# Kernel optimization log

Measured on AMD Instinct MI355X. Metric: run time of the kernel, lower is better.

Reference implementation:

```python
import jax, jax.numpy as jnp
import numpy as np

N = 50000    # nodes
E = 800000   # edges per block
D = 128      # embed_dim
H = 8        # heads
DH = D // H  # head dim
L = 2        # layers / blocks
IN = 128     # in_feats
P = 8192     # pos/neg pairs
FF = 2 * D   # FFN hidden
NEG_SLOPE = 0.2


def layer_norm(x, g, b, eps=1e-5):
    m = x.mean(-1, keepdims=True)
    v = ((x - m) ** 2).mean(-1, keepdims=True)
    return (x - m) / jnp.sqrt(v + eps) * g + b


def setup_inputs() -> dict:
    key = jax.random.key(0)
    ks = jax.random.split(key, 32)
    f32 = jnp.float32
    def w(k, shape, fan_in):
        return jax.random.normal(k, shape, f32) * (1.0 / np.sqrt(fan_in))
    inp = {
        'x': jax.random.normal(ks[0], (N, IN), f32),
        'src': jax.random.randint(ks[1], (L, E), 0, N),
        'dst': jax.random.randint(ks[2], (L, E), 0, N),
        'pos_src': jax.random.randint(ks[3], (P,), 0, N),
        'pos_dst': jax.random.randint(ks[4], (P,), 0, N),
        'neg_src': jax.random.randint(ks[5], (P,), 0, N),
        'neg_dst': jax.random.randint(ks[6], (P,), 0, N),
        # input projection
        'W_in': w(ks[7], (IN, D), IN), 'b_in': jnp.zeros((D,), f32),
        # per-layer attention weights, stacked over L
        'Wq': w(ks[8], (L, D, D), D), 'bq': jnp.zeros((L, D), f32),
        'Wk': w(ks[9], (L, D, D), D), 'bk': jnp.zeros((L, D), f32),
        'Wv': w(ks[10], (L, D, D), D), 'bv': jnp.zeros((L, D), f32),
        'Wo': w(ks[11], (L, D, D), D), 'bo': jnp.zeros((L, D), f32),
        'ln1_g': jnp.ones((L, D), f32), 'ln1_b': jnp.zeros((L, D), f32),
        'Wf1': w(ks[12], (L, D, FF), D), 'bf1': jnp.zeros((L, FF), f32),
        'Wf2': w(ks[13], (L, FF, D), FF), 'bf2': jnp.zeros((L, D), f32),
        'ln2_g': jnp.ones((L, D), f32), 'ln2_b': jnp.zeros((L, D), f32),
        # predictor MLP: D -> D//2 -> 1
        'Wp1': w(ks[14], (D, D // 2), D), 'bp1': jnp.zeros((D // 2,), f32),
        'Wp2': w(ks[15], (D // 2, 1), D // 2), 'bp2': jnp.zeros((1,), f32),
    }
    return inp


def reference(x, src, dst, pos_src, pos_dst, neg_src, neg_dst,
              W_in, b_in, Wq, bq, Wk, bk, Wv, bv, Wo, bo,
              ln1_g, ln1_b, Wf1, bf1, Wf2, bf2, ln2_g, ln2_b,
              Wp1, bp1, Wp2, bp2):
    scale = 1.0 / np.sqrt(DH)
    h = x @ W_in + b_in  # [N, D] (dropout is identity in eval mode)
    for l in range(L):
        s_l, d_l = src[l], dst[l]
        q = (h @ Wq[l] + bq[l]).reshape(N, H, DH)
        k = (h @ Wk[l] + bk[l]).reshape(N, H, DH)
        v = (h @ Wv[l] + bv[l]).reshape(N, H, DH)
        # per-edge attention scores [E, H]
        sc = jnp.einsum('ehd,ehd->eh', q[d_l], k[s_l]) * scale
        # segment softmax over incoming edges of each dst node
        m = jax.ops.segment_max(sc, d_l, num_segments=N)   # [N, H]
        ex = jnp.exp(sc - m[d_l])
        den = jax.ops.segment_sum(ex, d_l, num_segments=N)  # [N, H]
        alpha = ex / (den[d_l] + 1e-9)
        agg = jax.ops.segment_sum(alpha[..., None] * v[s_l], d_l,
                                  num_segments=N).reshape(N, D)
        h = layer_norm(h + agg @ Wo[l] + bo[l], ln1_g[l], ln1_b[l])
        ff = jax.nn.relu(h @ Wf1[l] + bf1[l]) @ Wf2[l] + bf2[l]
        h = layer_norm(h + ff, ln2_g[l], ln2_b[l])

    def predict(a, b):
        z = h[a] * h[b]  # gather-multiply edge scoring
        z = jax.nn.leaky_relu(z @ Wp1 + bp1, NEG_SLOPE)
        return z @ Wp2 + bp2  # [P, 1]

    pos_score = predict(pos_src, pos_dst)
    neg_score = predict(neg_src, neg_dst)
    return (pos_score, neg_score, h)
```

## Files before the change

### kernel.cpp

```cpp
#include <hip/hip_runtime.h>
#include <hip/hip_bf16.h>
#include <math.h>

#define N_NODES 50000
#define NE      800000
#define D       128
#define H       8
#define DH      16
#define NLAYER  2
#define IN_F    128
#define PP      8192
#define FF      256
#define MPAD    50048
#define CAP     96
#define NBIN    196
#define BCAP    48
#define GCAP    4608
#define CHUNK   2048

typedef short  bf16x8 __attribute__((ext_vector_type(8)));
typedef float  f32x4  __attribute__((ext_vector_type(4)));
typedef __hip_bfloat16 bf16;
typedef unsigned short u16;
typedef unsigned int   u32;

__device__ __forceinline__ float bflo(u32 u) { return __uint_as_float(u << 16); }
__device__ __forceinline__ float bfhi(u32 u) { return __uint_as_float(u & 0xffff0000u); }

__global__ __launch_bounds__(256) void bin_kernel(
    const int* __restrict__ dst, const int* __restrict__ src,
    u32* __restrict__ gbin, int* __restrict__ gbin_cnt)
{
    __shared__ u32 ent[NBIN * BCAP];
    __shared__ int bcnt[NBIN];
    const int t = threadIdx.x, l = blockIdx.y;
    const int base = blockIdx.x * CHUNK;
    if (t < NBIN) bcnt[t] = 0;
    __syncthreads();
    #pragma unroll
    for (int j = 0; j < CHUNK / 256; j++) {
        int e = base + j * 256 + t;
        if (e < NE) {
            int d = dst[(size_t)l * NE + e];
            int s = src[(size_t)l * NE + e];
            int bin = d >> 8;
            int slot = atomicAdd(&bcnt[bin], 1);
            if (slot < BCAP) ent[bin * BCAP + slot] = ((u32)s << 16) | (u32)(d & 255);
        }
    }
    __syncthreads();
    if (t < NBIN) {
        int c = bcnt[t]; if (c > BCAP) c = BCAP;
        if (c > 0) {
            int gb = atomicAdd(&gbin_cnt[l * NBIN + t], c);
            u32* gp = gbin + ((size_t)l * NBIN + t) * GCAP;
            for (int i = 0; i < c; i++)
                if (gb + i < GCAP) gp[gb + i] = ent[t * BCAP + i];
        }
    }
}

__global__ __launch_bounds__(256) void expand_kernel(
    const u32* __restrict__ gbin, const int* __restrict__ gbin_cnt,
    int* __restrict__ cnt, u16* __restrict__ ssrc)
{
    __shared__ int lcnt[256];
    const int t = threadIdx.x, b = blockIdx.x, l = blockIdx.y;
    lcnt[t] = 0;
    __syncthreads();
    int n = gbin_cnt[l * NBIN + b]; if (n > GCAP) n = GCAP;
    const u32* gp = gbin + ((size_t)l * NBIN + b) * GCAP;
    for (int i = t; i < n; i += 256) {
        u32 u = gp[i];
        int dl = (int)(u & 255);
        int pos = atomicAdd(&lcnt[dl], 1);
        if (pos < CAP) {
            int d = (b << 8) + dl;
            ssrc[((size_t)l * N_NODES + d) * CAP + pos] = (u16)(u >> 16);
        }
    }
    __syncthreads();
    int d = (b << 8) + t;
    if (d < N_NODES) cnt[l * N_NODES + d] = lcnt[t];
}

__global__ void xb_kernel(const float* __restrict__ x, bf16* __restrict__ xb) {
    int id = blockIdx.x * blockDim.x + threadIdx.x;
    if (id >= MPAD * IN_F) return;
    int r = id / IN_F;
    xb[id] = __float2bfloat16(r < N_NODES ? x[id] : 0.f);
}

__global__ void prep_kernel(const float* __restrict__ W_in,
                            const float* __restrict__ Wq, const float* __restrict__ Wk,
                            const float* __restrict__ Wv, const float* __restrict__ Wo,
                            const float* __restrict__ Wf1, const float* __restrict__ Wf2,
                            const float* __restrict__ bq, const float* __restrict__ bk,
                            const float* __restrict__ bv,
                            bf16* __restrict__ win_t, bf16* __restrict__ wqkv_t,
                            bf16* __restrict__ wo_t, bf16* __restrict__ wf1_t,
                            bf16* __restrict__ wf2_t, float* __restrict__ bqkv)
{
    int id = blockIdx.x * blockDim.x + threadIdx.x;
    if (id < 16384) {
        int n = id >> 7, k = id & 127;
        win_t[id] = __float2bfloat16(W_in[k * 128 + n]);
        return;
    }
    id -= 16384;
    if (id < NLAYER * 49152) {
        int l = id / 49152, j = id % 49152;
        int r = j >> 7, k = j & 127;
        const float* Ws; int col;
        if (r < 128) { Ws = Wq; col = r; }
        else {
            int u = r - 128, hh = u >> 5, w = u & 31;
            if (w < 16) { Ws = Wk; col = hh * 16 + w; }
            else        { Ws = Wv; col = hh * 16 + w - 16; }
        }
        wqkv_t[(size_t)l * 49152 + j] = __float2bfloat16(Ws[(size_t)l * 16384 + k * 128 + col]);
        return;
    }
    id -= NLAYER * 49152;
    if (id < NLAYER * 16384) {
        int l = id / 16384, j = id % 16384;
        int n = j >> 7, k = j & 127;
        wo_t[id] = __float2bfloat16(Wo[(size_t)l * 16384 + k * 128 + n]);
        return;
    }
    id -= NLAYER * 16384;
    if (id < NLAYER * 32768) {
        int l = id / 32768, j = id % 32768;
        int n = j >> 7, k = j & 127;
        wf1_t[id] = __float2bfloat16(Wf1[(size_t)l * 32768 + k * 256 + n]);
        return;
    }
    id -= NLAYER * 32768;
    if (id < NLAYER * 32768) {
        int l = id / 32768, j = id % 32768;
        int n = j >> 8, k = j & 255;
        wf2_t[id] = __float2bfloat16(Wf2[(size_t)l * 32768 + k * 128 + n]);
        return;
    }
    id -= NLAYER * 32768;
    if (id < NLAYER * 384) {
        int l = id / 384, r = id % 384;
        float v;
        if (r < 128) v = bq[l * 128 + r];
        else {
            int u = r - 128, hh = u >> 5, w = u & 31;
            v = (w < 16) ? bk[l * 128 + hh * 16 + w] : bv[l * 128 + hh * 16 + w - 16];
        }
        bqkv[l * 384 + r] = v;
    }
}

__global__ __launch_bounds__(256) void gemm_mfma(
    const bf16* __restrict__ A, const bf16* __restrict__ Wt,
    const float* __restrict__ bias,
    float* __restrict__ Cf, bf16* __restrict__ Cb,
    int Mvalid, int K, int Nc, int lda, int relu)
{
    __shared__ float4 As4[1024];
    __shared__ float4 Bs4[1024];
    char* As = (char*)As4;
    char* Bs = (char*)Bs4;
    const int t = threadIdx.x;
    const int wave = t >> 6, lane = t & 63;
    const int wr = wave >> 1, wc = wave & 1;
    const int r0 = blockIdx.x * 128, c0 = blockIdx.y * 128;

    f32x4 acc[4][4] = {};

    const int lrow   = t >> 3;
    const int lcol16 = (t & 7) * 16;

    for (int k0 = 0; k0 < K; k0 += 64) {
        #pragma unroll
        for (int p = 0; p < 4; p++) {
            int row = p * 32 + lrow;
            float4 av = *(const float4*)((const char*)(A  + (size_t)(r0 + row) * lda + k0) + lcol16);
            float4 bv = *(const float4*)((const char*)(Wt + (size_t)(c0 + row) * K + k0) + lcol16);
            int sw = lcol16 ^ ((row & 7) << 4);
            *(float4*)(As + row * 128 + sw) = av;
            *(float4*)(Bs + row * 128 + sw) = bv;
        }
        __syncthreads();
        #pragma unroll
        for (int kk = 0; kk < 2; kk++) {
            bf16x8 af[4], bfr[4];
            int kbyte = kk * 64 + (lane >> 4) * 16;
            #pragma unroll
            for (int m = 0; m < 4; m++) {
                int rowa = wr * 64 + m * 16 + (lane & 15);
                af[m]  = *(const bf16x8*)(As + rowa * 128 + (kbyte ^ ((rowa & 7) << 4)));
                int rowb = wc * 64 + m * 16 + (lane & 15);
                bfr[m] = *(const bf16x8*)(Bs + rowb * 128 + (kbyte ^ ((rowb & 7) << 4)));
            }
            #pragma unroll
            for (int m = 0; m < 4; m++)
                #pragma unroll
                for (int n = 0; n < 4; n++)
                    acc[m][n] = __builtin_amdgcn_mfma_f32_16x16x32_bf16(af[m], bfr[n], acc[m][n], 0, 0, 0);
        }
        __syncthreads();
    }

    const int colbase = c0 + wc * 64 + (lane & 15);
    const int rowbase = r0 + wr * 64 + ((lane >> 4) << 2);
    #pragma unroll
    for (int n = 0; n < 4; n++) {
        int col = colbase + n * 16;
        float bsv = bias[col];
        #pragma unroll
        for (int m = 0; m < 4; m++) {
            #pragma unroll
            for (int i = 0; i < 4; i++) {
                int row = rowbase + m * 16 + i;
                if (row < Mvalid) {
                    float v = acc[m][n][i] + bsv;
                    if (relu) v = fmaxf(v, 0.f);
                    if (Cf) Cf[(size_t)row * Nc + col] = v;
                    if (Cb) Cb[(size_t)row * Nc + col] = __float2bfloat16(v);
                }
            }
        }
    }
}

__global__ __launch_bounds__(256) void tail_fused(
    const bf16* __restrict__ qkv,
    const bf16* __restrict__ wo_t,
    const float* __restrict__ bo,
    const float* __restrict__ g1, const float* __restrict__ be1,
    const bf16* __restrict__ Wf1t,
    const float* __restrict__ b1,
    const bf16* __restrict__ Wf2t,
    const float* __restrict__ b2,
    const float* __restrict__ g2, const float* __restrict__ be2,
    float* __restrict__ h, bf16* __restrict__ hb)
{
    __shared__ char lds[81920];
    char* AsA = lds;
    char* Ah1 = lds;
    char* Xs  = lds + 16384;
    char* Bs  = lds + 49152;
    const int t = threadIdx.x;
    const int w = t >> 6, lane = t & 63;
    const int r0 = blockIdx.x * 64;
    const int c = lane & 15, sub = lane >> 4;

    f32x4 acc0[8] = {};
    #pragma unroll
    for (int k0 = 0; k0 < 128; k0 += 64) {
        {
            int row = t >> 2;
            int c16 = (t & 3) * 32;
            const char* ap = (const char*)(qkv + (size_t)(r0 + row) * 384 + k0);
            float4 a0 = *(const float4*)(ap + c16);
            float4 a1 = *(const float4*)(ap + c16 + 16);
            *(float4*)(AsA + row * 128 + ((c16)      ^ ((row & 7) << 4))) = a0;
            *(float4*)(AsA + row * 128 + ((c16 + 16) ^ ((row & 7) << 4))) = a1;
        }
        {
            int row = t >> 1;
            int c16 = (t & 1) * 64;
            const char* bp = (const char*)(wo_t + (size_t)row * 128 + k0);
            #pragma unroll
            for (int j = 0; j < 4; j++) {
                float4 b = *(const float4*)(bp + c16 + j * 16);
                *(float4*)(Bs + row * 128 + ((c16 + j * 16) ^ ((row & 7) << 4))) = b;
            }
        }
        __syncthreads();
        #pragma unroll
        for (int kk = 0; kk < 2; kk++) {
            int kbyte = kk * 64 + sub * 16;
            int rowa = w * 16 + c;
            bf16x8 af = *(const bf16x8*)(AsA + rowa * 128 + (kbyte ^ ((rowa & 7) << 4)));
            #pragma unroll
            for (int n = 0; n < 8; n++) {
                int rowb = n * 16 + c;
                bf16x8 bf8 = *(const bf16x8*)(Bs + rowb * 128 + (kbyte ^ ((rowb & 7) << 4)));
                acc0[n] = __builtin_amdgcn_mfma_f32_16x16x32_bf16(af, bf8, acc0[n], 0, 0, 0);
            }
        }
        __syncthreads();
    }

    float h1v[8][4];
    {
        float bsv[8], gv[8], bev[8];
        #pragma unroll
        for (int n = 0; n < 8; n++) {
            int col = n * 16 + c;
            bsv[n] = bo[col]; gv[n] = g1[col]; bev[n] = be1[col];
        }
        #pragma unroll
        for (int i = 0; i < 4; i++) {
            int row = r0 + w * 16 + sub * 4 + i;
            bool ok = row < N_NODES;
            float x[8];
            float s = 0.f;
            #pragma unroll
            for (int n = 0; n < 8; n++) {
                float res = ok ? h[(size_t)row * D + n * 16 + c] : 0.f;
                x[n] = res + acc0[n][i] + bsv[n];
                s += x[n];
            }
            s += __shfl_xor(s, 1); s += __shfl_xor(s, 2);
            s += __shfl_xor(s, 4); s += __shfl_xor(s, 8);
            float mean = s * (1.f / 128.f);
            float v = 0.f;
            #pragma unroll
            for (int n = 0; n < 8; n++) { float dd = x[n] - mean; v += dd * dd; }
            v += __shfl_xor(v, 1); v += __shfl_xor(v, 2);
            v += __shfl_xor(v, 4); v += __shfl_xor(v, 8);
            float rstd = rsqrtf(v * (1.f / 128.f) + 1e-5f);
            int lrow = w * 16 + sub * 4 + i;
            #pragma unroll
            for (int n = 0; n < 8; n++) {
                float o = (x[n] - mean) * rstd * gv[n] + bev[n];
                h1v[n][i] = o;
                int byte = (n * 16 + c) * 2;
                int addr = lrow * 256 + ((byte & ~15) ^ ((lrow & 7) << 4)) + (byte & 15);
                *(bf16*)(Ah1 + addr) = __float2bfloat16(o);
            }
        }
    }
    __syncthreads();

    f32x4 acc1[16] = {};
    #pragma unroll
    for (int kc = 0; kc < 2; kc++) {
        {
            int row = t;
            const char* bp = (const char*)Wf1t + row * 256 + kc * 128;
            #pragma unroll
            for (int j = 0; j < 8; j++) {
                float4 v = *(const float4*)(bp + j * 16);
                *(float4*)(Bs + row * 128 + ((j * 16) ^ ((row & 7) << 4))) = v;
            }
        }
        __syncthreads();
        #pragma unroll
        for (int kkl = 0; kkl < 2; kkl++) {
            int abyte = (kc * 2 + kkl) * 64 + sub * 16;
            int rowa = w * 16 + c;
            bf16x8 af = *(const bf16x8*)(Ah1 + rowa * 256 + (abyte ^ ((rowa & 7) << 4)));
            int bbyte = kkl * 64 + sub * 16;
            #pragma unroll
            for (int n = 0; n < 16; n++) {
                int rowb = n * 16 + c;
                bf16x8 bf8 = *(const bf16x8*)(Bs + rowb * 128 + (bbyte ^ ((rowb & 7) << 4)));
                acc1[n] = __builtin_amdgcn_mfma_f32_16x16x32_bf16(af, bf8, acc1[n], 0, 0, 0);
            }
        }
        __syncthreads();
    }

    #pragma unroll
    for (int n = 0; n < 16; n++) {
        float bs = b1[n * 16 + c];
        #pragma unroll
        for (int i = 0; i < 4; i++) {
            int row = w * 16 + sub * 4 + i;
            float v = fmaxf(acc1[n][i] + bs, 0.f);
            int byte = (n * 16 + c) * 2;
            int addr = row * 512 + ((byte & ~15) ^ ((row & 7) << 4)) + (byte & 15);
            *(bf16*)(Xs + addr) = __float2bfloat16(v);
        }
    }
    __syncthreads();

    f32x4 acc2[8] = {};
    #pragma unroll
    for (int kc = 0; kc < 2; kc++) {
        {
            int row = t >> 1;
            int off = (t & 1) * 128;
            const char* bp = (const char*)Wf2t + row * 512 + kc * 256 + off;
            #pragma unroll
            for (int j = 0; j < 8; j++) {
                float4 v = *(const float4*)(bp + j * 16);
                *(float4*)(Bs + row * 256 + ((off + j * 16) ^ ((row & 7) << 4))) = v;
            }
        }
        __syncthreads();
        #pragma unroll
        for (int kkl = 0; kkl < 4; kkl++) {
            int xbyte = kc * 256 + kkl * 64 + sub * 16;
            int rowa = w * 16 + c;
            bf16x8 af = *(const bf16x8*)(Xs + rowa * 512 + (xbyte ^ ((rowa & 7) << 4)));
            int bbyte = kkl * 64 + sub * 16;
            #pragma unroll
            for (int n = 0; n < 8; n++) {
                int rowb = n * 16 + c;
                bf16x8 bf8 = *(const bf16x8*)(Bs + rowb * 256 + (bbyte ^ ((rowb & 7) << 4)));
                acc2[n] = __builtin_amdgcn_mfma_f32_16x16x32_bf16(af, bf8, acc2[n], 0, 0, 0);
            }
        }
        __syncthreads();
    }

    {
        float bsv[8], gv[8], bev[8];
        #pragma unroll
        for (int n = 0; n < 8; n++) {
            int col = n * 16 + c;
            bsv[n] = b2[col]; gv[n] = g2[col]; bev[n] = be2[col];
        }
        #pragma unroll
        for (int i = 0; i < 4; i++) {
            int row = r0 + w * 16 + sub * 4 + i;
            bool ok = row < N_NODES;
            float x[8];
            float s = 0.f;
            #pragma unroll
            for (int n = 0; n < 8; n++) {
                x[n] = h1v[n][i] + acc2[n][i] + bsv[n];
                s += x[n];
            }
            s += __shfl_xor(s, 1); s += __shfl_xor(s, 2);
            s += __shfl_xor(s, 4); s += __shfl_xor(s, 8);
            float mean = s * (1.f / 128.f);
            float v = 0.f;
            #pragma unroll
            for (int n = 0; n < 8; n++) { float dd = x[n] - mean; v += dd * dd; }
            v += __shfl_xor(v, 1); v += __shfl_xor(v, 2);
            v += __shfl_xor(v, 4); v += __shfl_xor(v, 8);
            float rstd = rsqrtf(v * (1.f / 128.f) + 1e-5f);
            if (ok) {
                #pragma unroll
                for (int n = 0; n < 8; n++) {
                    float o = (x[n] - mean) * rstd * gv[n] + bev[n];
                    h [(size_t)row * D + n * 16 + c] = o;
                    hb[(size_t)row * D + n * 16 + c] = __float2bfloat16(o);
                }
            }
        }
    }
}

__global__ __launch_bounds__(256) void attn_fused(
    const bf16* __restrict__ qkv,
    const int* __restrict__ cnt, const u16* __restrict__ ssrc,
    bf16* __restrict__ aggout)
{
    const float S2 = 0.25f * 1.44269504088896f;
    int wid = threadIdx.x >> 6, lane = threadIdx.x & 63;
    int d = blockIdx.x * 4 + wid;
    if (d >= N_NODES) return;
    int slot = lane >> 3, h = lane & 7;

    const u32* qr = (const u32*)(qkv + (size_t)d * 384 + h * DH);
    float qf[16];
    {
        uint4 q0 = *(const uint4*)(qr);
        uint4 q1 = *(const uint4*)(qr + 4);
        qf[0]=bflo(q0.x); qf[1]=bfhi(q0.x); qf[2]=bflo(q0.y); qf[3]=bfhi(q0.y);
        qf[4]=bflo(q0.z); qf[5]=bfhi(q0.z); qf[6]=bflo(q0.w); qf[7]=bfhi(q0.w);
        qf[8]=bflo(q1.x); qf[9]=bfhi(q1.x); qf[10]=bflo(q1.y); qf[11]=bfhi(q1.y);
        qf[12]=bflo(q1.z); qf[13]=bfhi(q1.z); qf[14]=bflo(q1.w); qf[15]=bfhi(q1.w);
    }

    int deg = cnt[d];
    if (deg > CAP) deg = CAP;
    const u16* bp = ssrc + (size_t)d * CAP;
    float m2 = -INFINITY, den = 0.f;
    float acc[16] = {};

    for (int i = slot; i < deg; i += 8) {
        int s = bp[i];
        const uint4* kvp = (const uint4*)(qkv + (size_t)s * 384 + 128 + h * 32);
        uint4 k0 = kvp[0], k1 = kvp[1], v0 = kvp[2], v1 = kvp[3];
        float p = qf[0]*bflo(k0.x) + qf[1]*bfhi(k0.x)
                + qf[2]*bflo(k0.y) + qf[3]*bfhi(k0.y)
                + qf[4]*bflo(k0.z) + qf[5]*bfhi(k0.z)
                + qf[6]*bflo(k0.w) + qf[7]*bfhi(k0.w)
                + qf[8]*bflo(k1.x) + qf[9]*bfhi(k1.x)
                + qf[10]*bflo(k1.y) + qf[11]*bfhi(k1.y)
                + qf[12]*bflo(k1.z) + qf[13]*bfhi(k1.z)
                + qf[14]*bflo(k1.w) + qf[15]*bfhi(k1.w);
        float p2 = p * S2;
        float w;
        if (p2 > m2 + 8.f) {
            float f = exp2f(m2 - p2);
            den *= f;
            #pragma unroll
            for (int j = 0; j < 16; j++) acc[j] *= f;
            m2 = p2;
            w = 1.f;
        } else {
            w = exp2f(p2 - m2);
        }
        den += w;
        acc[0]  += w*bflo(v0.x); acc[1]  += w*bfhi(v0.x);
        acc[2]  += w*bflo(v0.y); acc[3]  += w*bfhi(v0.y);
        acc[4]  += w*bflo(v0.z); acc[5]  += w*bfhi(v0.z);
        acc[6]  += w*bflo(v0.w); acc[7]  += w*bfhi(v0.w);
        acc[8]  += w*bflo(v1.x); acc[9]  += w*bfhi(v1.x);
        acc[10] += w*bflo(v1.y); acc[11] += w*bfhi(v1.y);
        acc[12] += w*bflo(v1.z); acc[13] += w*bfhi(v1.z);
        acc[14] += w*bflo(v1.w); acc[15] += w*bfhi(v1.w);
    }

    #pragma unroll
    for (int o = 8; o < 64; o <<= 1) {
        float om   = __shfl_xor(m2, o);
        float oden = __shfl_xor(den, o);
        float M = fmaxf(m2, om);
        float fa = (m2 > -INFINITY) ? exp2f(m2 - M) : 0.f;
        float fb = (om > -INFINITY) ? exp2f(om - M) : 0.f;
        den = den * fa + oden * fb;
        #pragma unroll
        for (int j = 0; j < 16; j++) {
            float oa = __shfl_xor(acc[j], o);
            acc[j] = acc[j] * fa + oa * fb;
        }
        m2 = M;
    }

    float r = 1.f / (den + 1e-9f);
    float o0 = 0.f, o1 = 0.f;
    #pragma unroll
    for (int j = 0; j < 8; j++) {
        if (slot == j) { o0 = acc[2 * j]; o1 = acc[2 * j + 1]; }
    }
    bf16* op = aggout + (size_t)d * 384 + h * DH + slot * 2;
    op[0] = __float2bfloat16(o0 * r);
    op[1] = __float2bfloat16(o1 * r);
}

__global__ void predict_kernel(const float* __restrict__ h,
                               const int* __restrict__ ps, const int* __restrict__ pd,
                               const int* __restrict__ ns, const int* __restrict__ nd,
                               const float* __restrict__ Wp1, const float* __restrict__ bp1,
                               const float* __restrict__ Wp2, const float* __restrict__ bp2,
                               float* __restrict__ out)
{
    __shared__ float z[128];
    int p = blockIdx.x;
    int a, b;
    if (p < PP) { a = ps[p]; b = pd[p]; }
    else        { a = ns[p - PP]; b = nd[p - PP]; }
    int t = threadIdx.x;
    z[t]      = h[(size_t)a * D + t]      * h[(size_t)b * D + t];
    z[t + 64] = h[(size_t)a * D + t + 64] * h[(size_t)b * D + t + 64];
    __syncthreads();
    float acc = bp1[t];
    #pragma unroll 4
    for (int i = 0; i < 128; i++) acc += z[i] * Wp1[(size_t)i * 64 + t];
    acc = acc > 0.f ? acc : 0.2f * acc;
    float part = acc * Wp2[t];
    #pragma unroll
    for (int o = 32; o > 0; o >>= 1) part += __shfl_down(part, o);
    if (t == 0) out[p] = part + bp2[0];
}

extern "C" void kernel_launch(void* const* d_in, const int* in_sizes, int n_in,
                              void* d_out, int out_size, void* d_ws, size_t ws_size,
                              hipStream_t stream)
{
    const float* x       = (const float*)d_in[0];
    const int*   src     = (const int*)d_in[1];
    const int*   dst     = (const int*)d_in[2];
    const int*   pos_src = (const int*)d_in[3];
    const int*   pos_dst = (const int*)d_in[4];
    const int*   neg_src = (const int*)d_in[5];
    const int*   neg_dst = (const int*)d_in[6];
    const float* W_in = (const float*)d_in[7];
    const float* b_in = (const float*)d_in[8];
    const float* Wq = (const float*)d_in[9];
    const float* bq = (const float*)d_in[10];
    const float* Wk = (const float*)d_in[11];
    const float* bk = (const float*)d_in[12];
    const float* Wv = (const float*)d_in[13];
    const float* bv = (const float*)d_in[14];
    const float* Wo = (const float*)d_in[15];
    const float* bo = (const float*)d_in[16];
    const float* ln1g = (const float*)d_in[17];
    const float* ln1b = (const float*)d_in[18];
    const float* Wf1 = (const float*)d_in[19];
    const float* bf1 = (const float*)d_in[20];
    const float* Wf2 = (const float*)d_in[21];
    const float* bf2 = (const float*)d_in[22];
    const float* ln2g = (const float*)d_in[23];
    const float* ln2b = (const float*)d_in[24];
    const float* Wp1 = (const float*)d_in[25];
    const float* bp1 = (const float*)d_in[26];
    const float* Wp2 = (const float*)d_in[27];
    const float* bp2 = (const float*)d_in[28];

    float* out = (float*)d_out;
    float* h   = out + 2 * PP;

    bf16* B    = (bf16*)d_ws;
    bf16* qkvb = B;
    bf16* xb   = B;
    bf16* hb   = B + (size_t)MPAD * 384;
    int*  cnt  = (int*)(hb + (size_t)MPAD * 128);
    u16*  ssrc = (u16*)(cnt + 2 * N_NODES);
    bf16* wtb  = (bf16*)(ssrc + (size_t)2 * N_NODES * CAP);
    bf16* win_t  = wtb;
    bf16* wqkv_t = wtb + 16384;
    bf16* wo_t   = wtb + 16384 + 98304;
    bf16* wf1_t  = wtb + 16384 + 98304 + 32768;
    bf16* wf2_t  = wtb + 16384 + 98304 + 32768 + 65536;
    float* bqkv  = (float*)(wtb + 16384 + 98304 + 32768 + 65536 + 65536);
    int*  gbin_cnt = (int*)(bqkv + NLAYER * 384);
    u32*  gbin     = (u32*)(gbin_cnt + 2 * NBIN);

    auto cdiv = [](int a, int b) { return (a + b - 1) / b; };
    const int GX = MPAD / 128;
    const int GL = MPAD / 64;

    xb_kernel<<<cdiv(MPAD * IN_F, 256), 256, 0, stream>>>(x, xb);
    prep_kernel<<<1091, 256, 0, stream>>>(W_in, Wq, Wk, Wv, Wo, Wf1, Wf2, bq, bk, bv,
                                          win_t, wqkv_t, wo_t, wf1_t, wf2_t, bqkv);

    (void)hipMemsetAsync(gbin_cnt, 0, 2 * NBIN * sizeof(int), stream);
    bin_kernel<<<dim3(cdiv(NE, CHUNK), 2), 256, 0, stream>>>(dst, src, gbin, gbin_cnt);
    expand_kernel<<<dim3(NBIN, 2), 256, 0, stream>>>(gbin, gbin_cnt, cnt, ssrc);

    gemm_mfma<<<dim3(GX, 1), 256, 0, stream>>>(xb, win_t, b_in, h, hb, N_NODES, 128, 128, 128, 0);

    for (int l = 0; l < NLAYER; l++) {
        gemm_mfma<<<dim3(GX, 3), 256, 0, stream>>>(hb, wqkv_t + l * 49152, bqkv + l * 384,
                                                   nullptr, qkvb, N_NODES, 128, 384, 128, 0);

        attn_fused<<<cdiv(N_NODES, 4), 256, 0, stream>>>(qkvb, cnt + l * N_NODES,
                                                         ssrc + (size_t)l * N_NODES * CAP, qkvb);

        tail_fused<<<GL, 256, 0, stream>>>(qkvb, wo_t + l * 16384, bo + l * D,
                                           ln1g + l * D, ln1b + l * D,
                                           wf1_t + l * 32768, bf1 + l * FF,
                                           wf2_t + l * 32768, bf2 + l * D,
                                           ln2g + l * D, ln2b + l * D, h, hb);
    }

    predict_kernel<<<2 * PP, 64, 0, stream>>>(h, pos_src, pos_dst, neg_src, neg_dst,
                                              Wp1, bp1, Wp2, bp2, out);
}
```

Baseline: 362.0 us.

## Fuse input projection and QKV GEMMs into head and tail kernels

Adds a head kernel that converts x to bf16 in LDS, runs the input projection, and feeds the result straight into the layer-0 QKV projection. The tail kernel now computes the next layer's QKV from its LayerNorm output held in LDS. This removes the x-to-bf16 pass, the hb round trip through global memory and the standalone QKV GEMM launches. It also folds the bin-count memset into the prep kernel. The trade-off is more serial work and LDS per block, and the tail kernel now overwrites the qkv buffer it also reads from.

```diff
diff --git a/kernel.cpp b/kernel.cpp
--- a/kernel.cpp
+++ b/kernel.cpp
@@ -26,6 +26,7 @@
 
 __device__ __forceinline__ float bflo(u32 u) { return __uint_as_float(u << 16); }
 __device__ __forceinline__ float bfhi(u32 u) { return __uint_as_float(u & 0xffff0000u); }
+__device__ __forceinline__ u16 bfbits(float f) { bf16 t = __float2bfloat16(f); return *(u16*)&t; }
 
 __global__ __launch_bounds__(256) void bin_kernel(
     const int* __restrict__ dst, const int* __restrict__ src,
@@ -84,13 +85,6 @@
     if (d < N_NODES) cnt[l * N_NODES + d] = lcnt[t];
 }
 
-__global__ void xb_kernel(const float* __restrict__ x, bf16* __restrict__ xb) {
-    int id = blockIdx.x * blockDim.x + threadIdx.x;
-    if (id >= MPAD * IN_F) return;
-    int r = id / IN_F;
-    xb[id] = __float2bfloat16(r < N_NODES ? x[id] : 0.f);
-}
-
 __global__ void prep_kernel(const float* __restrict__ W_in,
                             const float* __restrict__ Wq, const float* __restrict__ Wk,
                             const float* __restrict__ Wv, const float* __restrict__ Wo,
@@ -99,7 +93,8 @@
                             const float* __restrict__ bv,
                             bf16* __restrict__ win_t, bf16* __restrict__ wqkv_t,
                             bf16* __restrict__ wo_t, bf16* __restrict__ wf1_t,
-                            bf16* __restrict__ wf2_t, float* __restrict__ bqkv)
+                            bf16* __restrict__ wf2_t, float* __restrict__ bqkv,
+                            int* __restrict__ gbin_cnt)
 {
     int id = blockIdx.x * blockDim.x + threadIdx.x;
     if (id < 16384) {
@@ -152,79 +147,127 @@
             v = (w < 16) ? bk[l * 128 + hh * 16 + w] : bv[l * 128 + hh * 16 + w - 16];
         }
         bqkv[l * 384 + r] = v;
-    }
+        return;
+    }
+    id -= NLAYER * 384;
+    if (id < 2 * NBIN) gbin_cnt[id] = 0;
 }
 
-__global__ __launch_bounds__(256) void gemm_mfma(
-    const bf16* __restrict__ A, const bf16* __restrict__ Wt,
-    const float* __restrict__ bias,
-    float* __restrict__ Cf, bf16* __restrict__ Cb,
-    int Mvalid, int K, int Nc, int lda, int relu)
+__global__ __launch_bounds__(256) void head_fused(
+    const float* __restrict__ x, const bf16* __restrict__ win_t,
+    const float* __restrict__ b_in,
+    const bf16* __restrict__ wqkv0, const float* __restrict__ bqkv0,
+    float* __restrict__ h, bf16* __restrict__ qkvb)
 {
-    __shared__ float4 As4[1024];
-    __shared__ float4 Bs4[1024];
-    char* As = (char*)As4;
-    char* Bs = (char*)Bs4;
+    __shared__ char lds[65536];
+    char* Axb = lds;
+    char* Hb  = lds + 16384;
+    char* Bs  = lds + 32768;
     const int t = threadIdx.x;
-    const int wave = t >> 6, lane = t & 63;
-    const int wr = wave >> 1, wc = wave & 1;
-    const int r0 = blockIdx.x * 128, c0 = blockIdx.y * 128;
-
-    f32x4 acc[4][4] = {};
-
-    const int lrow   = t >> 3;
-    const int lcol16 = (t & 7) * 16;
-
-    for (int k0 = 0; k0 < K; k0 += 64) {
-        #pragma unroll
-        for (int p = 0; p < 4; p++) {
-            int row = p * 32 + lrow;
-            float4 av = *(const float4*)((const char*)(A  + (size_t)(r0 + row) * lda + k0) + lcol16);
-            float4 bv = *(const float4*)((const char*)(Wt + (size_t)(c0 + row) * K + k0) + lcol16);
-            int sw = lcol16 ^ ((row & 7) << 4);
-            *(float4*)(As + row * 128 + sw) = av;
-            *(float4*)(Bs + row * 128 + sw) = bv;
+    const int w = t >> 6, lane = t & 63;
+    const int r0 = blockIdx.x * 64;
+    const int c = lane & 15, sub = lane >> 4;
+
+    {
+        int row = t >> 2;
+        int col0 = (t & 3) * 32;
+        int grow = r0 + row;
+        #pragma unroll
+        for (int j = 0; j < 8; j++) {
+            float4 v = make_float4(0.f, 0.f, 0.f, 0.f);
+            if (grow < N_NODES) v = *(const float4*)(x + (size_t)grow * 128 + col0 + j * 4);
+            u32 lo = ((u32)bfbits(v.y) << 16) | bfbits(v.x);
+            u32 hi = ((u32)bfbits(v.w) << 16) | bfbits(v.z);
+            int byte = (col0 + j * 4) * 2;
+            int addr = row * 256 + ((byte & ~15) ^ ((row & 7) << 4)) + (byte & 15);
+            *(u32*)(Axb + addr)     = lo;
+            *(u32*)(Axb + addr + 4) = hi;
+        }
+    }
+    {
+        int row = t >> 1;
+        int off = (t & 1) * 128;
+        const char* bp = (const char*)win_t + row * 256 + off;
+        #pragma unroll
+        for (int j = 0; j < 8; j++) {
+            float4 v = *(const float4*)(bp + j * 16);
+            *(float4*)(Bs + row * 256 + ((off + j * 16) ^ ((row & 7) << 4))) = v;
+        }
+    }
+    __syncthreads();
+
+    f32x4 acc0[8] = {};
+    #pragma unroll
+    for (int kc = 0; kc < 2; kc++) {
+        #pragma unroll
+        for (int kk = 0; kk < 2; kk++) {
+            int kbyte = (kc * 2 + kk) * 64 + sub * 16;
+            int rowa = w * 16 + c;
+            bf16x8 af = *(const bf16x8*)(Axb + rowa * 256 + (kbyte ^ ((rowa & 7) << 4)));
+            #pragma unroll
+            for (int n = 0; n < 8; n++) {
+                int rowb = n * 16 + c;
+                bf16x8 bf8 = *(const bf16x8*)(Bs + rowb * 256 + (kbyte ^ ((rowb & 7) << 4)));
+                acc0[n] = __builtin_amdgcn_mfma_f32_16x16x32_bf16(af, bf8, acc0[n], 0, 0, 0);
+            }
+        }
+    }
+
+    #pragma unroll
+    for (int i = 0; i < 4; i++) {
+        int lrow = w * 16 + sub * 4 + i;
+        int grow = r0 + lrow;
+        bool ok = grow < N_NODES;
+        #pragma unroll
+        for (int n = 0; n < 8; n++) {
+            float v = acc0[n][i] + b_in[n * 16 + c];
+            if (ok) h[(size_t)grow * D + n * 16 + c] = v;
+            int byte = (n * 16 + c) * 2;
+            int addr = lrow * 256 + ((byte & ~15) ^ ((lrow & 7) << 4)) + (byte & 15);
+            *(u16*)(Hb + addr) = bfbits(v);
+        }
+    }
+    __syncthreads();
+
+    #pragma unroll
+    for (int cc = 0; cc < 3; cc++) {
+        {
+            int row = t >> 1;
+            int off = (t & 1) * 128;
+            const char* bp = (const char*)wqkv0 + (size_t)(cc * 128 + row) * 256 + off;
+            #pragma unroll
+            for (int j = 0; j < 8; j++) {
+                float4 v = *(const float4*)(bp + j * 16);
+                *(float4*)(Bs + row * 256 + ((off + j * 16) ^ ((row & 7) << 4))) = v;
+            }
         }
         __syncthreads();
-        #pragma unroll
-        for (int kk = 0; kk < 2; kk++) {
-            bf16x8 af[4], bfr[4];
-            int kbyte = kk * 64 + (lane >> 4) * 16;
-            #pragma unroll
-            for (int m = 0; m < 4; m++) {
-                int rowa = wr * 64 + m * 16 + (lane & 15);
-                af[m]  = *(const bf16x8*)(As + rowa * 128 + (kbyte ^ ((rowa & 7) << 4)));
-                int rowb = wc * 64 + m * 16 + (lane & 15);
-                bfr[m] = *(const bf16x8*)(Bs + rowb * 128 + (kbyte ^ ((rowb & 7) << 4)));
-            }
-            #pragma unroll
-            for (int m = 0; m < 4; m++)
+        f32x4 acc[8] = {};
+        #pragma unroll
+        for (int kc = 0; kc < 2; kc++) {
+            #pragma unroll
+            for (int kk = 0; kk < 2; kk++) {
+                int kbyte = (kc * 2 + kk) * 64 + sub * 16;
+                int rowa = w * 16 + c;
+                bf16x8 af = *(const bf16x8*)(Hb + rowa * 256 + (kbyte ^ ((rowa & 7) << 4)));
                 #pragma unroll
-                for (int n = 0; n < 4; n++)
-                    acc[m][n] = __builtin_amdgcn_mfma_f32_16x16x32_bf16(af[m], bfr[n], acc[m][n], 0, 0, 0);
+                for (int n = 0; n < 8; n++) {
+                    int rowb = n * 16 + c;
+                    bf16x8 bf8 = *(const bf16x8*)(Bs + rowb * 256 + (kbyte ^ ((rowb & 7) << 4)));
+                    acc[n] = __builtin_amdgcn_mfma_f32_16x16x32_bf16(af, bf8, acc[n], 0, 0, 0);
+                }
+            }
+        }
+        #pragma unroll
+        for (int i = 0; i < 4; i++) {
+            int grow = r0 + w * 16 + sub * 4 + i;
+            #pragma unroll
+            for (int n = 0; n < 8; n++) {
+                int col = cc * 128 + n * 16 + c;
+                qkvb[(size_t)grow * 384 + col] = __float2bfloat16(acc[n][i] + bqkv0[col]);
+            }
         }
         __syncthreads();
-    }
-
-    const int colbase = c0 + wc * 64 + (lane & 15);
-    const int rowbase = r0 + wr * 64 + ((lane >> 4) << 2);
-    #pragma unroll
-    for (int n = 0; n < 4; n++) {
-        int col = colbase + n * 16;
-        float bsv = bias[col];
-        #pragma unroll
-        for (int m = 0; m < 4; m++) {
-            #pragma unroll
-            for (int i = 0; i < 4; i++) {
-                int row = rowbase + m * 16 + i;
-                if (row < Mvalid) {
-                    float v = acc[m][n][i] + bsv;
-                    if (relu) v = fmaxf(v, 0.f);
-                    if (Cf) Cf[(size_t)row * Nc + col] = v;
-                    if (Cb) Cb[(size_t)row * Nc + col] = __float2bfloat16(v);
-                }
-            }
-        }
     }
 }
 
@@ -238,7 +281,9 @@
     const bf16* __restrict__ Wf2t,
     const float* __restrict__ b2,
     const float* __restrict__ g2, const float* __restrict__ be2,
-    float* __restrict__ h, bf16* __restrict__ hb)
+    float* __restrict__ h,
+    const bf16* __restrict__ wqkv_next, const float* __restrict__ bqkv_next,
+    bf16* __restrict__ qkvb_out)
 {
     __shared__ char lds[81920];
     char* AsA = lds;
@@ -324,7 +369,7 @@
                 h1v[n][i] = o;
                 int byte = (n * 16 + c) * 2;
                 int addr = lrow * 256 + ((byte & ~15) ^ ((lrow & 7) << 4)) + (byte & 15);
-                *(bf16*)(Ah1 + addr) = __float2bfloat16(o);
+                *(u16*)(Ah1 + addr) = bfbits(o);
             }
         }
     }
@@ -368,7 +413,7 @@
             float v = fmaxf(acc1[n][i] + bs, 0.f);
             int byte = (n * 16 + c) * 2;
             int addr = row * 512 + ((byte & ~15) ^ ((row & 7) << 4)) + (byte & 15);
-            *(bf16*)(Xs + addr) = __float2bfloat16(v);
+            *(u16*)(Xs + addr) = bfbits(v);
         }
     }
     __syncthreads();
@@ -412,8 +457,9 @@
         }
         #pragma unroll
         for (int i = 0; i < 4; i++) {
-            int row = r0 + w * 16 + sub * 4 + i;
-            bool ok = row < N_NODES;
+            int lrow = w * 16 + sub * 4 + i;
+            int grow = r0 + lrow;
+            bool ok = grow < N_NODES;
             float x[8];
             float s = 0.f;
             #pragma unroll
@@ -430,14 +476,57 @@
             v += __shfl_xor(v, 1); v += __shfl_xor(v, 2);
             v += __shfl_xor(v, 4); v += __shfl_xor(v, 8);
             float rstd = rsqrtf(v * (1.f / 128.f) + 1e-5f);
-            if (ok) {
+            #pragma unroll
+            for (int n = 0; n < 8; n++) {
+                float o = (x[n] - mean) * rstd * gv[n] + bev[n];
+                if (ok) h[(size_t)grow * D + n * 16 + c] = o;
+                int byte = (n * 16 + c) * 2;
+                int addr = lrow * 256 + ((byte & ~15) ^ ((lrow & 7) << 4)) + (byte & 15);
+                *(u16*)(Xs + addr) = bfbits(o);
+            }
+        }
+    }
+
+    if (wqkv_next) {
+        #pragma unroll
+        for (int cc = 0; cc < 3; cc++) {
+            {
+                int row = t >> 1;
+                int off = (t & 1) * 128;
+                const char* bp = (const char*)wqkv_next + (size_t)(cc * 128 + row) * 256 + off;
+                #pragma unroll
+                for (int j = 0; j < 8; j++) {
+                    float4 v = *(const float4*)(bp + j * 16);
+                    *(float4*)(Bs + row * 256 + ((off + j * 16) ^ ((row & 7) << 4))) = v;
+                }
+            }
+            __syncthreads();
+            f32x4 acc[8] = {};
+            #pragma unroll
+            for (int kc = 0; kc < 2; kc++) {
+                #pragma unroll
+                for (int kk = 0; kk < 2; kk++) {
+                    int kbyte = (kc * 2 + kk) * 64 + sub * 16;
+                    int rowa = w * 16 + c;
+                    bf16x8 af = *(const bf16x8*)(Xs + rowa * 256 + (kbyte ^ ((rowa & 7) << 4)));
+                    #pragma unroll
+                    for (int n = 0; n < 8; n++) {
+                        int rowb = n * 16 + c;
+                        bf16x8 bf8 = *(const bf16x8*)(Bs + rowb * 256 + (kbyte ^ ((rowb & 7) << 4)));
+                        acc[n] = __builtin_amdgcn_mfma_f32_16x16x32_bf16(af, bf8, acc[n], 0, 0, 0);
+                    }
+                }
+            }
+            #pragma unroll
+            for (int i = 0; i < 4; i++) {
+                int grow = r0 + w * 16 + sub * 4 + i;
                 #pragma unroll
                 for (int n = 0; n < 8; n++) {
-                    float o = (x[n] - mean) * rstd * gv[n] + bev[n];
-                    h [(size_t)row * D + n * 16 + c] = o;
-                    hb[(size_t)row * D + n * 16 + c] = __float2bfloat16(o);
+                    int col = cc * 128 + n * 16 + c;
+                    qkvb_out[(size_t)grow * 384 + col] = __float2bfloat16(acc[n][i] + bqkv_next[col]);
                 }
             }
+            __syncthreads();
         }
     }
 }
@@ -597,9 +686,7 @@
 
     bf16* B    = (bf16*)d_ws;
     bf16* qkvb = B;
-    bf16* xb   = B;
-    bf16* hb   = B + (size_t)MPAD * 384;
-    int*  cnt  = (int*)(hb + (size_t)MPAD * 128);
+    int*  cnt  = (int*)(B + (size_t)MPAD * 384);
     u16*  ssrc = (u16*)(cnt + 2 * N_NODES);
     bf16* wtb  = (bf16*)(ssrc + (size_t)2 * N_NODES * CAP);
     bf16* win_t  = wtb;
@@ -612,31 +699,26 @@
     u32*  gbin     = (u32*)(gbin_cnt + 2 * NBIN);
 
     auto cdiv = [](int a, int b) { return (a + b - 1) / b; };
-    const int GX = MPAD / 128;
     const int GL = MPAD / 64;
 
-    xb_kernel<<<cdiv(MPAD * IN_F, 256), 256, 0, stream>>>(x, xb);
-    prep_kernel<<<1091, 256, 0, stream>>>(W_in, Wq, Wk, Wv, Wo, Wf1, Wf2, bq, bk, bv,
-                                          win_t, wqkv_t, wo_t, wf1_t, wf2_t, bqkv);
-
-    (void)hipMemsetAsync(gbin_cnt, 0, 2 * NBIN * sizeof(int), stream);
+    prep_kernel<<<1093, 256, 0, stream>>>(W_in, Wq, Wk, Wv, Wo, Wf1, Wf2, bq, bk, bv,
+                                          win_t, wqkv_t, wo_t, wf1_t, wf2_t, bqkv, gbin_cnt);
     bin_kernel<<<dim3(cdiv(NE, CHUNK), 2), 256, 0, stream>>>(dst, src, gbin, gbin_cnt);
     expand_kernel<<<dim3(NBIN, 2), 256, 0, stream>>>(gbin, gbin_cnt, cnt, ssrc);
 
-    gemm_mfma<<<dim3(GX, 1), 256, 0, stream>>>(xb, win_t, b_in, h, hb, N_NODES, 128, 128, 128, 0);
+    head_fused<<<GL, 256, 0, stream>>>(x, win_t, b_in, wqkv_t, bqkv, h, qkvb);
 
     for (int l = 0; l < NLAYER; l++) {
-        gemm_mfma<<<dim3(GX, 3), 256, 0, stream>>>(hb, wqkv_t + l * 49152, bqkv + l * 384,
-                                                   nullptr, qkvb, N_NODES, 128, 384, 128, 0);
-
         attn_fused<<<cdiv(N_NODES, 4), 256, 0, stream>>>(qkvb, cnt + l * N_NODES,
                                                          ssrc + (size_t)l * N_NODES * CAP, qkvb);
-
+        const bf16* wnext  = (l + 1 < NLAYER) ? (wqkv_t + (l + 1) * 49152) : nullptr;
+        const float* bnext = (l + 1 < NLAYER) ? (bqkv + (l + 1) * 384) : nullptr;
         tail_fused<<<GL, 256, 0, stream>>>(qkvb, wo_t + l * 16384, bo + l * D,
                                            ln1g + l * D, ln1b + l * D,
                                            wf1_t + l * 32768, bf1 + l * FF,
                                            wf2_t + l * 32768, bf2 + l * D,
-                                           ln2g + l * D, ln2b + l * D, h, hb);
+                                           ln2g + l * D, ln2b + l * D, h,
+                                           wnext, bnext, qkvb);
     }
 
     predict_kernel<<<2 * PP, 64, 0, stream>>>(h, pos_src, pos_dst, neg_src, neg_dst,
```

Result: slower. 406.9 us (+12.4%).

## Split FFN hidden dimension into halves to shrink tail kernel LDS footprint

Applied to the files above, without the earlier changes.

The fused tail kernel's FFN now processes the 256-wide hidden layer in two 128-column halves. Each half is computed, passed through ReLU, and immediately accumulated into the second GEMM, so the hidden-activation buffer and weight staging buffers shrink and total LDS drops from 80 KB to 48 KB. This is meant to allow more resident blocks per CU, at the cost of more barriers and smaller weight tiles per stage. Separately, the gbin_cnt memset is folded into prep_kernel to remove one API call.

```diff
diff --git a/kernel.cpp b/kernel.cpp
--- a/kernel.cpp
+++ b/kernel.cpp
@@ -26,6 +26,7 @@
 
 __device__ __forceinline__ float bflo(u32 u) { return __uint_as_float(u << 16); }
 __device__ __forceinline__ float bfhi(u32 u) { return __uint_as_float(u & 0xffff0000u); }
+__device__ __forceinline__ u16 bfbits(float f) { bf16 t = __float2bfloat16(f); return *(u16*)&t; }
 
 __global__ __launch_bounds__(256) void bin_kernel(
     const int* __restrict__ dst, const int* __restrict__ src,
@@ -99,7 +100,8 @@
                             const float* __restrict__ bv,
                             bf16* __restrict__ win_t, bf16* __restrict__ wqkv_t,
                             bf16* __restrict__ wo_t, bf16* __restrict__ wf1_t,
-                            bf16* __restrict__ wf2_t, float* __restrict__ bqkv)
+                            bf16* __restrict__ wf2_t, float* __restrict__ bqkv,
+                            int* __restrict__ gbin_cnt)
 {
     int id = blockIdx.x * blockDim.x + threadIdx.x;
     if (id < 16384) {
@@ -152,7 +154,10 @@
             v = (w < 16) ? bk[l * 128 + hh * 16 + w] : bv[l * 128 + hh * 16 + w - 16];
         }
         bqkv[l * 384 + r] = v;
-    }
+        return;
+    }
+    id -= NLAYER * 384;
+    if (id < 2 * NBIN) gbin_cnt[id] = 0;
 }
 
 __global__ __launch_bounds__(256) void gemm_mfma(
@@ -240,11 +245,11 @@
     const float* __restrict__ g2, const float* __restrict__ be2,
     float* __restrict__ h, bf16* __restrict__ hb)
 {
-    __shared__ char lds[81920];
+    __shared__ char lds[49152];
     char* AsA = lds;
     char* Ah1 = lds;
     char* Xs  = lds + 16384;
-    char* Bs  = lds + 49152;
+    char* Bs  = lds + 32768;
     const int t = threadIdx.x;
     const int w = t >> 6, lane = t & 63;
     const int r0 = blockIdx.x * 64;
@@ -324,83 +329,84 @@
                 h1v[n][i] = o;
                 int byte = (n * 16 + c) * 2;
                 int addr = lrow * 256 + ((byte & ~15) ^ ((lrow & 7) << 4)) + (byte & 15);
-                *(bf16*)(Ah1 + addr) = __float2bfloat16(o);
-            }
-        }
-    }
-    __syncthreads();
-
-    f32x4 acc1[16] = {};
-    #pragma unroll
-    for (int kc = 0; kc < 2; kc++) {
-        {
-            int row = t;
-            const char* bp = (const char*)Wf1t + row * 256 + kc * 128;
-            #pragma unroll
-            for (int j = 0; j < 8; j++) {
-                float4 v = *(const float4*)(bp + j * 16);
-                *(float4*)(Bs + row * 128 + ((j * 16) ^ ((row & 7) << 4))) = v;
-            }
-        }
-        __syncthreads();
-        #pragma unroll
-        for (int kkl = 0; kkl < 2; kkl++) {
-            int abyte = (kc * 2 + kkl) * 64 + sub * 16;
-            int rowa = w * 16 + c;
-            bf16x8 af = *(const bf16x8*)(Ah1 + rowa * 256 + (abyte ^ ((rowa & 7) << 4)));
-            int bbyte = kkl * 64 + sub * 16;
-            #pragma unroll
-            for (int n = 0; n < 16; n++) {
-                int rowb = n * 16 + c;
-                bf16x8 bf8 = *(const bf16x8*)(Bs + rowb * 128 + (bbyte ^ ((rowb & 7) << 4)));
-                acc1[n] = __builtin_amdgcn_mfma_f32_16x16x32_bf16(af, bf8, acc1[n], 0, 0, 0);
-            }
-        }
-        __syncthreads();
-    }
-
-    #pragma unroll
-    for (int n = 0; n < 16; n++) {
-        float bs = b1[n * 16 + c];
-        #pragma unroll
-        for (int i = 0; i < 4; i++) {
-            int row = w * 16 + sub * 4 + i;
-            float v = fmaxf(acc1[n][i] + bs, 0.f);
-            int byte = (n * 16 + c) * 2;
-            int addr = row * 512 + ((byte & ~15) ^ ((row & 7) << 4)) + (byte & 15);
-            *(bf16*)(Xs + addr) = __float2bfloat16(v);
+                *(u16*)(Ah1 + addr) = bfbits(o);
+            }
         }
     }
     __syncthreads();
 
     f32x4 acc2[8] = {};
     #pragma unroll
-    for (int kc = 0; kc < 2; kc++) {
-        {
-            int row = t >> 1;
-            int off = (t & 1) * 128;
-            const char* bp = (const char*)Wf2t + row * 512 + kc * 256 + off;
-            #pragma unroll
-            for (int j = 0; j < 8; j++) {
-                float4 v = *(const float4*)(bp + j * 16);
-                *(float4*)(Bs + row * 256 + ((off + j * 16) ^ ((row & 7) << 4))) = v;
+    for (int xh = 0; xh < 2; xh++) {
+        f32x4 acc1[8] = {};
+        #pragma unroll
+        for (int kc = 0; kc < 2; kc++) {
+            {
+                int row = t >> 1;
+                int off = (t & 1) * 64;
+                const char* bp = (const char*)Wf1t + (size_t)(xh * 128 + row) * 256 + kc * 128 + off;
+                #pragma unroll
+                for (int j = 0; j < 4; j++) {
+                    float4 v = *(const float4*)(bp + j * 16);
+                    *(float4*)(Bs + row * 128 + ((off + j * 16) ^ ((row & 7) << 4))) = v;
+                }
+            }
+            __syncthreads();
+            #pragma unroll
+            for (int kkl = 0; kkl < 2; kkl++) {
+                int abyte = (kc * 2 + kkl) * 64 + sub * 16;
+                int rowa = w * 16 + c;
+                bf16x8 af = *(const bf16x8*)(Ah1 + rowa * 256 + (abyte ^ ((rowa & 7) << 4)));
+                int bbyte = kkl * 64 + sub * 16;
+                #pragma unroll
+                for (int n = 0; n < 8; n++) {
+                    int rowb = n * 16 + c;
+                    bf16x8 bf8 = *(const bf16x8*)(Bs + rowb * 128 + (bbyte ^ ((rowb & 7) << 4)));
+                    acc1[n] = __builtin_amdgcn_mfma_f32_16x16x32_bf16(af, bf8, acc1[n], 0, 0, 0);
+                }
+            }
+            __syncthreads();
+        }
+        #pragma unroll
+        for (int n = 0; n < 8; n++) {
+            float bs = b1[xh * 128 + n * 16 + c];
+            #pragma unroll
+            for (int i = 0; i < 4; i++) {
+                int row = w * 16 + sub * 4 + i;
+                float v = fmaxf(acc1[n][i] + bs, 0.f);
+                int byte = (n * 16 + c) * 2;
+                int addr = row * 256 + ((byte & ~15) ^ ((row & 7) << 4)) + (byte & 15);
+                *(u16*)(Xs + addr) = bfbits(v);
             }
         }
         __syncthreads();
         #pragma unroll
-        for (int kkl = 0; kkl < 4; kkl++) {
-            int xbyte = kc * 256 + kkl * 64 + sub * 16;
-            int rowa = w * 16 + c;
-            bf16x8 af = *(const bf16x8*)(Xs + rowa * 512 + (xbyte ^ ((rowa & 7) << 4)));
-            int bbyte = kkl * 64 + sub * 16;
-            #pragma unroll
-            for (int n = 0; n < 8; n++) {
-                int rowb = n * 16 + c;
-                bf16x8 bf8 = *(const bf16x8*)(Bs + rowb * 256 + (bbyte ^ ((rowb & 7) << 4)));
-                acc2[n] = __builtin_amdgcn_mfma_f32_16x16x32_bf16(af, bf8, acc2[n], 0, 0, 0);
-            }
-        }
-        __syncthreads();
+        for (int oh = 0; oh < 2; oh++) {
+            {
+                int row = t >> 2;
+                int off = (t & 3) * 64;
+                const char* bp = (const char*)Wf2t + (size_t)(oh * 64 + row) * 512 + xh * 256 + off;
+                #pragma unroll
+                for (int j = 0; j < 4; j++) {
+                    float4 v = *(const float4*)(bp + j * 16);
+                    *(float4*)(Bs + row * 256 + ((off + j * 16) ^ ((row & 7) << 4))) = v;
+                }
+            }
+            __syncthreads();
+            #pragma unroll
+            for (int kkl = 0; kkl < 4; kkl++) {
+                int xbyte = kkl * 64 + sub * 16;
+                int rowa = w * 16 + c;
+                bf16x8 af = *(const bf16x8*)(Xs + rowa * 256 + (xbyte ^ ((rowa & 7) << 4)));
+                #pragma unroll
+                for (int n = 0; n < 4; n++) {
+                    int rowb = n * 16 + c;
+                    bf16x8 bf8 = *(const bf16x8*)(Bs + rowb * 256 + (xbyte ^ ((rowb & 7) << 4)));
+                    acc2[oh * 4 + n] = __builtin_amdgcn_mfma_f32_16x16x32_bf16(af, bf8, acc2[oh * 4 + n], 0, 0, 0);
+                }
+            }
+            __syncthreads();
+        }
     }
 
     {
@@ -616,10 +622,9 @@
     const int GL = MPAD / 64;
 
     xb_kernel<<<cdiv(MPAD * IN_F, 256), 256, 0, stream>>>(x, xb);
-    prep_kernel<<<1091, 256, 0, stream>>>(W_in, Wq, Wk, Wv, Wo, Wf1, Wf2, bq, bk, bv,
-                                          win_t, wqkv_t, wo_t, wf1_t, wf2_t, bqkv);
-
-    (void)hipMemsetAsync(gbin_cnt, 0, 2 * NBIN * sizeof(int), stream);
+    prep_kernel<<<1093, 256, 0, stream>>>(W_in, Wq, Wk, Wv, Wo, Wf1, Wf2, bq, bk, bv,
+                                          win_t, wqkv_t, wo_t, wf1_t, wf2_t, bqkv, gbin_cnt);
+
     bin_kernel<<<dim3(cdiv(NE, CHUNK), 2), 256, 0, stream>>>(dst, src, gbin, gbin_cnt);
     expand_kernel<<<dim3(NBIN, 2), 256, 0, stream>>>(gbin, gbin_cnt, cnt, ssrc);
 
```

New measurement: 349.6 us. 1.04x faster.
